# Kernel tuning notes

Hardware: AMD Instinct MI355X
Metric: run time of the kernel (lower is better)

## Reference

```python
import jax, jax.numpy as jnp
import numpy as np

N, E, F, H, C1 = 50000, 1_600_000, 48, 1, 16  # nodes, edges, in_feats, heads, conv out


def setup_inputs() -> dict:
    key = jax.random.key(0)
    ks = jax.random.split(key, 12)
    in_ = jax.random.normal(ks[0], (N, F), dtype=jnp.float32)
    edge_index = jax.random.randint(ks[1], (2, E), 0, N, dtype=jnp.int64)
    labels = jax.random.bernoulli(ks[2], 0.5, (N, 1)).astype(jnp.float32)
    weights = jax.random.uniform(ks[3], (N, 1), dtype=jnp.float32) + 0.5
    s = 0.1  # PyG FeaStConv init: normal(0, 0.1)
    W = jax.random.normal(ks[4], (F, H * C1), dtype=jnp.float32) * s
    u = jax.random.normal(ks[5], (F, H), dtype=jnp.float32) * s
    c = jax.random.normal(ks[6], (H,), dtype=jnp.float32) * s
    bias = jax.random.normal(ks[7], (C1,), dtype=jnp.float32) * s
    lin1_w = jax.random.normal(ks[8], (C1, 8), dtype=jnp.float32) * (1.0 / np.sqrt(C1))
    lin1_b = jnp.zeros((8,), dtype=jnp.float32)
    out_w = jax.random.normal(ks[9], (8, 1), dtype=jnp.float32) * (1.0 / np.sqrt(8))
    out_b = jnp.zeros((1,), dtype=jnp.float32)
    return {"in_": in_, "edge_index": edge_index, "labels": labels,
            "weights": weights, "W": W, "u": u, "c": c, "bias": bias,
            "lin1_w": lin1_w, "lin1_b": lin1_b, "out_w": out_w, "out_b": out_b}


def feast_conv(x, edge_index, W, u, c, bias):
    n = x.shape[0]
    loop = jnp.arange(n, dtype=edge_index.dtype)  # add_self_loops=True
    src = jnp.concatenate([edge_index[0], loop])
    dst = jnp.concatenate([edge_index[1], loop])
    xj = x[src]                                   # [E+N, F] gather
    xi = x[dst]
    q = jax.nn.softmax((xj - xi) @ u + c, axis=-1)            # [E+N, H]
    xw = (xj @ W).reshape(-1, H, C1)                           # [E+N, H, C1]
    msg = jnp.einsum('ehc,eh->ec', xw, q)                      # [E+N, C1]
    agg = jax.ops.segment_sum(msg, dst, num_segments=n)        # scatter-sum
    deg = jax.ops.segment_sum(jnp.ones_like(dst, dtype=x.dtype), dst, num_segments=n)
    return agg / jnp.maximum(deg, 1.0)[:, None] + bias         # mean aggregation


def reference(in_, edge_index, labels, weights, W, u, c, bias, lin1_w, lin1_b, out_w, out_b):
    x = jax.nn.relu(feast_conv(in_, edge_index, W, u, c, bias))
    x = jax.nn.relu(x @ lin1_w + lin1_b)
    p = jax.nn.sigmoid(x @ out_w + out_b)                      # [N, 1]
    eps = 1e-7
    pc = jnp.clip(p, eps, 1.0 - eps)
    bce = -(labels * jnp.log(pc) + (1.0 - labels) * jnp.log(1.0 - pc))
    loss = jnp.mean(weights * bce)
    return (loss, p)
```

## Files before the change

### kernel.cpp

```cpp
#include <hip/hip_runtime.h>

constexpr int N_NODES  = 50000;
constexpr int N_EDGES  = 1600000;
constexpr int F_IN     = 48;
constexpr int C1_OUT   = 16;

constexpr int BNODES    = 64;
constexpr int NBINS     = 782;
constexpr int FILL_BLKS = 256;
constexpr int EPB       = N_EDGES / FILL_BLKS;
constexpr int SCAP      = 16;
constexpr int OCAP      = 16384;
constexpr int BIN_INTS  = FILL_BLKS * SCAP;
constexpr int ROWCAP    = 98;
constexpr int XW_BLKS   = 49;

constexpr size_t OFLOW_OFF = 256;
constexpr size_t XW_OFF    = OFLOW_OFF + (size_t)OCAP * 4;
constexpr size_t GSLOT_OFF = XW_OFF + (size_t)N_NODES * C1_OUT * 4;

__device__ __forceinline__ void xw_body(int n, const float* __restrict__ x,
                                        const float* __restrict__ W,
                                        float* __restrict__ xw)
{
    const float4* xr = (const float4*)(x + (long)n * F_IN);
    float h[C1_OUT];
    #pragma unroll
    for (int c = 0; c < C1_OUT; ++c) h[c] = 0.f;
    #pragma unroll
    for (int k = 0; k < F_IN / 4; ++k) {
        float4 v = xr[k];
        #pragma unroll
        for (int c = 0; c < C1_OUT; ++c) {
            h[c] = fmaf(v.x, W[(4*k+0)*C1_OUT + c],
                   fmaf(v.y, W[(4*k+1)*C1_OUT + c],
                   fmaf(v.z, W[(4*k+2)*C1_OUT + c],
                   fmaf(v.w, W[(4*k+3)*C1_OUT + c], h[c]))));
        }
    }
    float4* o = (float4*)(xw + (long)n * C1_OUT);
    o[0] = make_float4(h[0],  h[1],  h[2],  h[3]);
    o[1] = make_float4(h[4],  h[5],  h[6],  h[7]);
    o[2] = make_float4(h[8],  h[9],  h[10], h[11]);
    o[3] = make_float4(h[12], h[13], h[14], h[15]);
}

__global__ __launch_bounds__(1024)
void k_fill_xw(const int* __restrict__ src, const int* __restrict__ dst,
               int* __restrict__ gslot, int* __restrict__ ocnt,
               unsigned int* __restrict__ oflow,
               const float* __restrict__ x, const float* __restrict__ W,
               float* __restrict__ xw)
{
    __shared__ int lcnt[NBINS];
    __shared__ int lstage[NBINS * SCAP];

    if (blockIdx.x >= FILL_BLKS) {
        int n = (blockIdx.x - FILL_BLKS) * 1024 + threadIdx.x;
        if (n < N_NODES) xw_body(n, x, W, xw);
        return;
    }

    int tid = threadIdx.x;
    if (tid < NBINS) lcnt[tid] = 0;
    __syncthreads();

    int e0 = blockIdx.x * EPB;
    for (int i = tid; i < EPB; i += 1024) {
        int e = e0 + i;
        int s = src[e], d = dst[e];
        int b = d >> 6;
        int p = atomicAdd(&lcnt[b], 1);
        if (p < SCAP) {
            lstage[(b << 4) + p] = (s << 6) | (d & 63);
        } else {
            int g = atomicAdd(ocnt, 1);
            if (g < OCAP) oflow[g] = ((unsigned)s << 16) | (unsigned)d;
        }
    }
    __syncthreads();

    for (int idx = tid; idx < NBINS * SCAP; idx += 1024) {
        int b = idx >> 4, s = idx & 15;
        int v = (s < lcnt[b]) ? lstage[idx] : -1;
        gslot[((size_t)b * FILL_BLKS + blockIdx.x) * SCAP + s] = v;
    }
}

__global__ __launch_bounds__(256)
void k_agg(const int* __restrict__ gslot, int* __restrict__ ctrl,
           const unsigned int* __restrict__ oflow, const float* __restrict__ xw,
           const float* __restrict__ bias, const float* __restrict__ lin1_w,
           const float* __restrict__ lin1_b, const float* __restrict__ out_w,
           const float* __restrict__ out_b, const float* __restrict__ labels,
           const float* __restrict__ weights, float* __restrict__ out)
{
    __shared__ int ndeg[BNODES];
    __shared__ unsigned short lrow[BNODES][ROWCAP];
    __shared__ float acc[BNODES][17];
    __shared__ float sLossW[4];

    int B = blockIdx.x, tid = threadIdx.x, lane = tid & 63, w = tid >> 6;

    if (tid < BNODES) ndeg[tid] = 0;
    __syncthreads();

    const int4* sp = (const int4*)(gslot + (size_t)B * BIN_INTS);
    int4 q0 = sp[tid], q1 = sp[tid + 256], q2 = sp[tid + 512], q3 = sp[tid + 768];

    int oc = ctrl[0]; if (oc > OCAP) oc = OCAP;

    #define SC1(v) if ((v) >= 0) { int ln = (v) & 63;               \
        int p = atomicAdd(&ndeg[ln], 1);                            \
        if (p < ROWCAP) lrow[ln][p] = (unsigned short)((unsigned)(v) >> 6); }
    SC1(q0.x); SC1(q0.y); SC1(q0.z); SC1(q0.w);
    SC1(q1.x); SC1(q1.y); SC1(q1.z); SC1(q1.w);
    SC1(q2.x); SC1(q2.y); SC1(q2.z); SC1(q2.w);
    SC1(q3.x); SC1(q3.y); SC1(q3.z); SC1(q3.w);
    #undef SC1
    for (int i = tid; i < oc; i += 256) {
        unsigned v = oflow[i];
        int d = (int)(v & 0xffffu);
        if ((d >> 6) == B) {
            int ln = d & 63;
            int p = atomicAdd(&ndeg[ln], 1);
            if (p < ROWCAP) lrow[ln][p] = (unsigned short)(v >> 16);
        }
    }
    __syncthreads();

    int rslot = lane >> 2, c4 = lane & 3;
    #pragma unroll
    for (int i = 0; i < 16; i += 2) {
        int ln0 = w * 16 + i, ln1 = ln0 + 1;
        int d0 = ndeg[ln0]; if (d0 > ROWCAP) d0 = ROWCAP;
        int d1 = ndeg[ln1]; if (d1 > ROWCAP) d1 = ROWCAP;
        int m = (d0 > d1) ? d0 : d1;
        float4 a0 = make_float4(0.f, 0.f, 0.f, 0.f);
        float4 a1 = make_float4(0.f, 0.f, 0.f, 0.f);
        for (int j0 = 0; j0 < m; j0 += 16) {
            int j = j0 + rslot;
            if (j < d0) {
                int s = lrow[ln0][j];
                float4 v = ((const float4*)(xw + (size_t)s * C1_OUT))[c4];
                a0.x += v.x; a0.y += v.y; a0.z += v.z; a0.w += v.w;
            }
            if (j < d1) {
                int s = lrow[ln1][j];
                float4 v = ((const float4*)(xw + (size_t)s * C1_OUT))[c4];
                a1.x += v.x; a1.y += v.y; a1.z += v.z; a1.w += v.w;
            }
        }
        #pragma unroll
        for (int off = 4; off < 64; off <<= 1) {
            a0.x += __shfl_xor(a0.x, off, 64);
            a1.x += __shfl_xor(a1.x, off, 64);
            a0.y += __shfl_xor(a0.y, off, 64);
            a1.y += __shfl_xor(a1.y, off, 64);
            a0.z += __shfl_xor(a0.z, off, 64);
            a1.z += __shfl_xor(a1.z, off, 64);
            a0.w += __shfl_xor(a0.w, off, 64);
            a1.w += __shfl_xor(a1.w, off, 64);
        }
        if (lane < 8) {
            int ln = (lane < 4) ? ln0 : ln1;
            float4 a = (lane < 4) ? a0 : a1;
            int c = lane & 3;
            acc[ln][c * 4 + 0] = a.x;
            acc[ln][c * 4 + 1] = a.y;
            acc[ln][c * 4 + 2] = a.z;
            acc[ln][c * 4 + 3] = a.w;
        }
    }

    float lossw = 0.f;
    if (lane < 16) {
        int ln = w * 16 + lane;
        int n = B * BNODES + ln;
        if (n < N_NODES) {
            int dg = ndeg[ln]; if (dg > ROWCAP) dg = ROWCAP;
            float inv = 1.f / (float)(dg + 1);
            const float4* xs4 = (const float4*)(xw + (size_t)n * C1_OUT);
            float xs[16];
            ((float4*)xs)[0] = xs4[0]; ((float4*)xs)[1] = xs4[1];
            ((float4*)xs)[2] = xs4[2]; ((float4*)xs)[3] = xs4[3];
            float h[16];
            #pragma unroll
            for (int c = 0; c < 16; ++c)
                h[c] = fmaxf(fmaf(acc[ln][c] + xs[c], inv, bias[c]), 0.f);
            float z = out_b[0];
            #pragma unroll
            for (int j = 0; j < 8; ++j) {
                float t = lin1_b[j];
                #pragma unroll
                for (int k = 0; k < 16; ++k) t = fmaf(h[k], lin1_w[k * 8 + j], t);
                z = fmaf(fmaxf(t, 0.f), out_w[j], z);
            }
            float p = 1.f / (1.f + __expf(-z));
            out[1 + n] = p;
            const float eps = 1e-7f;
            float pc = fminf(fmaxf(p, eps), 1.f - eps);
            float y  = labels[n];
            lossw = weights[n] * (-(y * __logf(pc) + (1.f - y) * __logf(1.f - pc)));
        }
    }
    lossw += __shfl_xor(lossw, 1, 64);
    lossw += __shfl_xor(lossw, 2, 64);
    lossw += __shfl_xor(lossw, 4, 64);
    lossw += __shfl_xor(lossw, 8, 64);
    if (lane == 0) sLossW[w] = lossw;
    __syncthreads();

    if (tid == 0) {
        float t = sLossW[0] + sLossW[1] + sLossW[2] + sLossW[3];
        float* loss_acc = (float*)&ctrl[2];
        atomicAdd(loss_acc, t);
        __threadfence();
        int r = atomicAdd(&ctrl[1], 1);
        if (r == NBINS - 1) {
            float total = atomicAdd(loss_acc, 0.f);
            out[0] = total / (float)N_NODES;
        }
    }
}

extern "C" void kernel_launch(void* const* d_in, const int* in_sizes, int n_in,
                              void* d_out, int out_size, void* d_ws, size_t ws_size,
                              hipStream_t stream)
{
    const float* x       = (const float*)d_in[0];
    const int*   eidx    = (const int*)  d_in[1];
    const float* labels  = (const float*)d_in[2];
    const float* weights = (const float*)d_in[3];
    const float* W       = (const float*)d_in[4];
    const float* bias    = (const float*)d_in[7];
    const float* lin1_w  = (const float*)d_in[8];
    const float* lin1_b  = (const float*)d_in[9];
    const float* out_w   = (const float*)d_in[10];
    const float* out_b   = (const float*)d_in[11];
    float* out = (float*)d_out;

    const int* src = eidx;
    const int* dst = eidx + N_EDGES;
    char* ws = (char*)d_ws;

    int*          ctrl  = (int*)ws;
    unsigned int* oflow = (unsigned int*)(ws + OFLOW_OFF);
    float*        xw    = (float*)(ws + XW_OFF);
    int*          gslot = (int*)(ws + GSLOT_OFF);

    hipMemsetAsync(ctrl, 0, 12, stream);
    k_fill_xw<<<FILL_BLKS + XW_BLKS, 1024, 0, stream>>>(
        src, dst, gslot, ctrl, oflow, x, W, xw);
    k_agg<<<NBINS, 256, 0, stream>>>(
        gslot, ctrl, oflow, xw, bias, lin1_w, lin1_b,
        out_w, out_b, labels, weights, out);
}
```

Before: 153.4 us.

## Split each aggregation bin across two blocks of 32 nodes

```diff
diff --git a/kernel.cpp b/kernel.cpp
--- a/kernel.cpp
+++ b/kernel.cpp
@@ -12,6 +12,8 @@
 constexpr int SCAP      = 16;
 constexpr int OCAP      = 16384;
 constexpr int BIN_INTS  = FILL_BLKS * SCAP;
+constexpr int HNODES    = 32;
+constexpr int AGG_BLKS  = NBINS * 2;
 constexpr int ROWCAP    = 98;
 constexpr int XW_BLKS   = 49;
 
@@ -95,14 +97,15 @@
            const float* __restrict__ out_b, const float* __restrict__ labels,
            const float* __restrict__ weights, float* __restrict__ out)
 {
-    __shared__ int ndeg[BNODES];
-    __shared__ unsigned short lrow[BNODES][ROWCAP];
-    __shared__ float acc[BNODES][17];
+    __shared__ int ndeg[HNODES];
+    __shared__ unsigned short lrow[HNODES][ROWCAP];
+    __shared__ float acc[HNODES][17];
     __shared__ float sLossW[4];
 
-    int B = blockIdx.x, tid = threadIdx.x, lane = tid & 63, w = tid >> 6;
-
-    if (tid < BNODES) ndeg[tid] = 0;
+    int B = blockIdx.x >> 1, H = blockIdx.x & 1;
+    int tid = threadIdx.x, lane = tid & 63, w = tid >> 6;
+
+    if (tid < HNODES) ndeg[tid] = 0;
     __syncthreads();
 
     const int4* sp = (const int4*)(gslot + (size_t)B * BIN_INTS);
@@ -110,8 +113,9 @@
 
     int oc = ctrl[0]; if (oc > OCAP) oc = OCAP;
 
-    #define SC1(v) if ((v) >= 0) { int ln = (v) & 63;               \
-        int p = atomicAdd(&ndeg[ln], 1);                            \
+    #define SC1(v) if ((v) >= 0 && ((((v) >> 5) & 1) == H)) {        \
+        int ln = (v) & 31;                                           \
+        int p = atomicAdd(&ndeg[ln], 1);                             \
         if (p < ROWCAP) lrow[ln][p] = (unsigned short)((unsigned)(v) >> 6); }
     SC1(q0.x); SC1(q0.y); SC1(q0.z); SC1(q0.w);
     SC1(q1.x); SC1(q1.y); SC1(q1.z); SC1(q1.w);
@@ -121,8 +125,8 @@
     for (int i = tid; i < oc; i += 256) {
         unsigned v = oflow[i];
         int d = (int)(v & 0xffffu);
-        if ((d >> 6) == B) {
-            int ln = d & 63;
+        if ((d >> 6) == B && (((d >> 5) & 1) == H)) {
+            int ln = d & 31;
             int p = atomicAdd(&ndeg[ln], 1);
             if (p < ROWCAP) lrow[ln][p] = (unsigned short)(v >> 16);
         }
@@ -131,41 +135,64 @@
 
     int rslot = lane >> 2, c4 = lane & 3;
     #pragma unroll
-    for (int i = 0; i < 16; i += 2) {
-        int ln0 = w * 16 + i, ln1 = ln0 + 1;
-        int d0 = ndeg[ln0]; if (d0 > ROWCAP) d0 = ROWCAP;
-        int d1 = ndeg[ln1]; if (d1 > ROWCAP) d1 = ROWCAP;
-        int m = (d0 > d1) ? d0 : d1;
+    for (int qd = 0; qd < 2; ++qd) {
+        int base = w * 8 + qd * 4;
+        int d0 = ndeg[base + 0]; if (d0 > ROWCAP) d0 = ROWCAP;
+        int d1 = ndeg[base + 1]; if (d1 > ROWCAP) d1 = ROWCAP;
+        int d2 = ndeg[base + 2]; if (d2 > ROWCAP) d2 = ROWCAP;
+        int d3 = ndeg[base + 3]; if (d3 > ROWCAP) d3 = ROWCAP;
+        int m01 = (d0 > d1) ? d0 : d1;
+        int m23 = (d2 > d3) ? d2 : d3;
+        int m = (m01 > m23) ? m01 : m23;
         float4 a0 = make_float4(0.f, 0.f, 0.f, 0.f);
-        float4 a1 = make_float4(0.f, 0.f, 0.f, 0.f);
+        float4 a1 = a0, a2 = a0, a3 = a0;
         for (int j0 = 0; j0 < m; j0 += 16) {
             int j = j0 + rslot;
             if (j < d0) {
-                int s = lrow[ln0][j];
+                int s = lrow[base + 0][j];
                 float4 v = ((const float4*)(xw + (size_t)s * C1_OUT))[c4];
                 a0.x += v.x; a0.y += v.y; a0.z += v.z; a0.w += v.w;
             }
             if (j < d1) {
-                int s = lrow[ln1][j];
+                int s = lrow[base + 1][j];
                 float4 v = ((const float4*)(xw + (size_t)s * C1_OUT))[c4];
                 a1.x += v.x; a1.y += v.y; a1.z += v.z; a1.w += v.w;
+            }
+            if (j < d2) {
+                int s = lrow[base + 2][j];
+                float4 v = ((const float4*)(xw + (size_t)s * C1_OUT))[c4];
+                a2.x += v.x; a2.y += v.y; a2.z += v.z; a2.w += v.w;
+            }
+            if (j < d3) {
+                int s = lrow[base + 3][j];
+                float4 v = ((const float4*)(xw + (size_t)s * C1_OUT))[c4];
+                a3.x += v.x; a3.y += v.y; a3.z += v.z; a3.w += v.w;
             }
         }
         #pragma unroll
         for (int off = 4; off < 64; off <<= 1) {
             a0.x += __shfl_xor(a0.x, off, 64);
             a1.x += __shfl_xor(a1.x, off, 64);
+            a2.x += __shfl_xor(a2.x, off, 64);
+            a3.x += __shfl_xor(a3.x, off, 64);
             a0.y += __shfl_xor(a0.y, off, 64);
             a1.y += __shfl_xor(a1.y, off, 64);
+            a2.y += __shfl_xor(a2.y, off, 64);
+            a3.y += __shfl_xor(a3.y, off, 64);
             a0.z += __shfl_xor(a0.z, off, 64);
             a1.z += __shfl_xor(a1.z, off, 64);
+            a2.z += __shfl_xor(a2.z, off, 64);
+            a3.z += __shfl_xor(a3.z, off, 64);
             a0.w += __shfl_xor(a0.w, off, 64);
             a1.w += __shfl_xor(a1.w, off, 64);
-        }
-        if (lane < 8) {
-            int ln = (lane < 4) ? ln0 : ln1;
-            float4 a = (lane < 4) ? a0 : a1;
+            a2.w += __shfl_xor(a2.w, off, 64);
+            a3.w += __shfl_xor(a3.w, off, 64);
+        }
+        if (lane < 16) {
+            int nd = lane >> 2;
+            float4 a = (nd == 0) ? a0 : (nd == 1) ? a1 : (nd == 2) ? a2 : a3;
             int c = lane & 3;
+            int ln = base + nd;
             acc[ln][c * 4 + 0] = a.x;
             acc[ln][c * 4 + 1] = a.y;
             acc[ln][c * 4 + 2] = a.z;
@@ -174,9 +201,9 @@
     }
 
     float lossw = 0.f;
-    if (lane < 16) {
-        int ln = w * 16 + lane;
-        int n = B * BNODES + ln;
+    if (lane < 8) {
+        int ln = w * 8 + lane;
+        int n = B * BNODES + H * HNODES + ln;
         if (n < N_NODES) {
             int dg = ndeg[ln]; if (dg > ROWCAP) dg = ROWCAP;
             float inv = 1.f / (float)(dg + 1);
@@ -207,7 +234,6 @@
     lossw += __shfl_xor(lossw, 1, 64);
     lossw += __shfl_xor(lossw, 2, 64);
     lossw += __shfl_xor(lossw, 4, 64);
-    lossw += __shfl_xor(lossw, 8, 64);
     if (lane == 0) sLossW[w] = lossw;
     __syncthreads();
 
@@ -217,7 +243,7 @@
         atomicAdd(loss_acc, t);
         __threadfence();
         int r = atomicAdd(&ctrl[1], 1);
-        if (r == NBINS - 1) {
+        if (r == AGG_BLKS - 1) {
             float total = atomicAdd(loss_acc, 0.f);
             out[0] = total / (float)N_NODES;
         }
@@ -252,7 +278,7 @@
     hipMemsetAsync(ctrl, 0, 12, stream);
     k_fill_xw<<<FILL_BLKS + XW_BLKS, 1024, 0, stream>>>(
         src, dst, gslot, ctrl, oflow, x, W, xw);
-    k_agg<<<NBINS, 256, 0, stream>>>(
+    k_agg<<<AGG_BLKS, 256, 0, stream>>>(
         gslot, ctrl, oflow, xw, bias, lin1_w, lin1_b,
         out_w, out_b, labels, weights, out);
 }
```

Result: slower. 171.9 us (+12.1%).
